# Kernel tuning notes

Measured on AMD Instinct MI355X. Metric: run time of the kernel, lower is better.

## Reference

```python
import jax, jax.numpy as jnp
import numpy as np

OUT_H, OUT_W = 512, 512
BATCH, CHANNELS = 64, 3


def setup_inputs() -> dict:
    key = jax.random.key(0)
    k1, k2 = jax.random.split(key)
    U = jax.random.normal(k1, (BATCH, OUT_H, OUT_W, CHANNELS), dtype=jnp.float32)
    theta = jax.random.normal(k2, (BATCH, 1), dtype=jnp.float32)
    return {"U": U, "theta": theta}


def reference(U, theta):
    B = U.shape[0]
    H, W = OUT_H, OUT_W
    # normalized sampling grid [H*W, 3] with homogeneous coordinate
    gx, gy = jnp.meshgrid(jnp.linspace(-1.0, 1.0, W), jnp.linspace(-1.0, 1.0, H))
    grid = jnp.stack([gx, gy, jnp.ones_like(gx)], axis=-1).reshape(H * W, 3)
    # rotation-only affine matrix [B, 2, 3]
    cos_t, sin_t, z = jnp.cos(theta), jnp.sin(theta), jnp.zeros_like(theta)
    rot = jnp.concatenate([cos_t, -sin_t, z, sin_t, cos_t, z], axis=1).reshape(B, 2, 3)
    # transformed source coords [B, H*W, 2]
    T_g = jnp.einsum('bij,nj->bni', rot, grid)
    x = (T_g[..., 0] + 1.0) * (W - 1) / 2.0
    y = (T_g[..., 1] + 1.0) * (H - 1) / 2.0
    x0f = jnp.floor(x).astype(jnp.int32)
    y0f = jnp.floor(y).astype(jnp.int32)
    x0 = jnp.clip(x0f, 0, W - 1)
    x1 = jnp.clip(x0f + 1, 0, W - 1)
    y0 = jnp.clip(y0f, 0, H - 1)
    y1 = jnp.clip(y0f + 1, 0, H - 1)
    # 4-corner gathers, batched: [B, H*W, C]
    gather = jax.vmap(lambda u, yy, xx: u[yy, xx])
    Ia = gather(U, y0, x0)
    Ib = gather(U, y1, x0)
    Ic = gather(U, y0, x1)
    Id = gather(U, y1, x1)
    x0_f, x1_f = x0.astype(jnp.float32), x1.astype(jnp.float32)
    y0_f, y1_f = y0.astype(jnp.float32), y1.astype(jnp.float32)
    wa = (x1_f - x) * (y1_f - y)
    wb = (x1_f - x) * (y - y0_f)
    wc = (x - x0_f) * (y1_f - y)
    wd = (x - x0_f) * (y - y0_f)
    out = (wa[..., None] * Ia + wb[..., None] * Ib
           + wc[..., None] * Ic + wd[..., None] * Id)
    return out.reshape(B, H, W, -1)
```

## Files before the change

### kernel.cpp

```cpp
#include <hip/hip_runtime.h>
#include <hip/hip_fp16.h>

#define OUT_H 512
#define OUT_W 512
#define BATCH 64
#define CHANS 3

#define WROWS 48
#define WPX   48
#define LPITCH 50
#define LSLOTS (WROWS * LPITCH)
#define IDX_MAX 2348

__global__ __launch_bounds__(256) void st_bilinear_kernel(
    const float* __restrict__ U,
    const float* __restrict__ theta,
    float* __restrict__ out)
{
    __shared__ __align__(16) unsigned int smA[LSLOTS];
    __shared__ __align__(16) unsigned int smB[LSLOTS];

    int blk  = blockIdx.x;
    int lblk = (blk & 7) * 2048 + (blk >> 3);

    int b  = lblk >> 8;
    int t  = lblk & 255;
    int i0 = (t >> 4) << 5;
    int j0 = (t & 15) << 5;

    int tid = threadIdx.x;

    float tt = theta[b];
    float s, c;
    __sincosf(tt, &s, &c);

    const float scale = 2.0f / 511.0f;
    float gx0 = (float)j0 * scale - 1.0f;
    float gy0 = (float)i0 * scale - 1.0f;
    float xb0 = (c * gx0 - s * gy0 + 1.0f) * 255.5f;
    float yb0 = (s * gx0 + c * gy0 + 1.0f) * 255.5f;

    float xmin = xb0 + fminf(0.0f, 31.0f * c) + fminf(0.0f, -31.0f * s);
    float ymin = yb0 + fminf(0.0f, 31.0f * s) + fminf(0.0f,  31.0f * c);

    int bx0 = min(max((int)floorf(xmin), 0), OUT_W - 1);
    int by0 = min(max((int)floorf(ymin), 0), OUT_H - 1);
    int bx_load = min(bx0, OUT_W - WPX);
    int by_load = min(by0, OUT_H - WROWS);

    const float* Ub = U + (size_t)b * (OUT_H * OUT_W * CHANS);
    const float* gb = Ub + ((size_t)by_load * OUT_W + bx_load) * CHANS;

    float4 va[5];
    float2 vb[5];
#pragma unroll
    for (int it = 0; it < 5; ++it) {
        unsigned P = (unsigned)tid + 256u * it;
        if (it < 4 || tid < 128) {
            unsigned r  = P / 24u;
            unsigned pr = P - r * 24u;
            const float* p = gb + (size_t)r * (OUT_W * CHANS) + pr * 6u;
            va[it] = *(const float4*)p;
            vb[it] = *(const float2*)(p + 4);
        }
    }
#pragma unroll
    for (int it = 0; it < 5; ++it) {
        unsigned P = (unsigned)tid + 256u * it;
        if (it < 4 || tid < 128) {
            unsigned r  = P / 24u;
            unsigned pr = P - r * 24u;
            unsigned slot = r * LPITCH + pr * 2u;
            float4 v = va[it]; float2 w = vb[it];
            __half2 ha0 = __floats2half2_rn(v.x, v.y);
            __half2 hb0 = __floats2half2_rn(v.z, 0.0f);
            __half2 ha1 = __floats2half2_rn(v.w, w.x);
            __half2 hb1 = __floats2half2_rn(w.y, 0.0f);
            uint2 wa, wb;
            wa.x = *(unsigned int*)&ha0; wa.y = *(unsigned int*)&ha1;
            wb.x = *(unsigned int*)&hb0; wb.y = *(unsigned int*)&hb1;
            *(uint2*)(smA + slot) = wa;
            *(uint2*)(smB + slot) = wb;
        }
    }
    __syncthreads();

    int il = tid >> 3;
    int jb = (tid & 7) << 2;
    float ilf = (float)il;
    float xr = xb0 - s * ilf;
    float yr = yb0 + c * ilf;
    int Koff = by_load * LPITCH + bx_load;

    float o[12];
#pragma unroll
    for (int p = 0; p < 4; ++p) {
        float jlf = (float)(jb + p);
        float x = fmaf(c, jlf, xr);
        float y = fmaf(s, jlf, yr);

        int ix = __float2int_rd(x);
        int iy = __float2int_rd(y);
        float fx = x - (float)ix;
        float fy = y - (float)iy;

        int idx = iy * LPITCH + ix - Koff;
        idx = min(max(idx, 0), IDX_MAX);

        unsigned iA0 = smA[idx],          iA1 = smA[idx + 1];
        unsigned iA2 = smA[idx + LPITCH], iA3 = smA[idx + LPITCH + 1];
        unsigned iB0 = smB[idx],          iB1 = smB[idx + 1];
        unsigned iB2 = smB[idx + LPITCH], iB3 = smB[idx + LPITCH + 1];

        __half2 fx2 = __float2half2_rn(fx);
        __half2 fy2 = __float2half2_rn(fy);
        __half2 A0 = *(__half2*)&iA0, A1 = *(__half2*)&iA1;
        __half2 A2 = *(__half2*)&iA2, A3 = *(__half2*)&iA3;
        __half2 B0 = *(__half2*)&iB0, B1 = *(__half2*)&iB1;
        __half2 B2 = *(__half2*)&iB2, B3 = *(__half2*)&iB3;

        __half2 tA = __hfma2(fx2, __hsub2(A1, A0), A0);
        __half2 bA = __hfma2(fx2, __hsub2(A3, A2), A2);
        __half2 rA = __hfma2(fy2, __hsub2(bA, tA), tA);
        __half2 tB = __hfma2(fx2, __hsub2(B1, B0), B0);
        __half2 bB = __hfma2(fx2, __hsub2(B3, B2), B2);
        __half2 rB = __hfma2(fy2, __hsub2(bB, tB), tB);

        bool valid = (x >= 0.0f) && (x < 511.0f) && (y >= 0.0f) && (y < 511.0f);
        o[p * 3 + 0] = valid ? __low2float(rA)  : 0.0f;
        o[p * 3 + 1] = valid ? __high2float(rA) : 0.0f;
        o[p * 3 + 2] = valid ? __low2float(rB)  : 0.0f;
    }

    float* po = out + (((size_t)b * OUT_H + (i0 + il)) * OUT_W + (j0 + jb)) * CHANS;
    ((float4*)po)[0] = make_float4(o[0], o[1], o[2],  o[3]);
    ((float4*)po)[1] = make_float4(o[4], o[5], o[6],  o[7]);
    ((float4*)po)[2] = make_float4(o[8], o[9], o[10], o[11]);
}

extern "C" void kernel_launch(void* const* d_in, const int* in_sizes, int n_in,
                              void* d_out, int out_size, void* d_ws, size_t ws_size,
                              hipStream_t stream) {
    const float* U     = (const float*)d_in[0];
    const float* theta = (const float*)d_in[1];
    float* out = (float*)d_out;

    int blocks = BATCH * (OUT_H / 32) * (OUT_W / 32);
    st_bilinear_kernel<<<blocks, 256, 0, stream>>>(U, theta, out);
}
```

Baseline: 103.4 us.

## Stage fp32 interleaved RGB tile in LDS instead of split fp16 planes

Replaces the two fp16 LDS planes (RG and B) with a single fp32 tile that keeps the interleaved RGB layout, using an odd pitch of 139 floats and a slightly smaller 46x46 window. The staging loop becomes plain float4 global loads written directly as scalars, with no half conversion or packing. Bilinear interpolation runs in fp32 from 12 scalar LDS reads per pixel. This drops conversion ALU work and the fp16 precision loss, at the cost of more LDS reads per pixel and a smaller halo margin for the rotated footprint. It also makes the batch index wave-uniform when loading theta.

Result: slower. 108.0 us (+4.5%).

```diff
diff --git a/kernel.cpp b/kernel.cpp
--- a/kernel.cpp
+++ b/kernel.cpp
@@ -1,24 +1,23 @@
 #include <hip/hip_runtime.h>
-#include <hip/hip_fp16.h>
 
 #define OUT_H 512
 #define OUT_W 512
 #define BATCH 64
 #define CHANS 3
 
-#define WROWS 48
-#define WPX   48
-#define LPITCH 50
-#define LSLOTS (WROWS * LPITCH)
-#define IDX_MAX 2348
+#define WROWS 46
+#define WPX   46
+#define RDW   138
+#define PITCH 139
+#define LSZ   (WROWS * PITCH)
+#define IDXMAX 6249
 
 __global__ __launch_bounds__(256) void st_bilinear_kernel(
     const float* __restrict__ U,
     const float* __restrict__ theta,
     float* __restrict__ out)
 {
-    __shared__ __align__(16) unsigned int smA[LSLOTS];
-    __shared__ __align__(16) unsigned int smB[LSLOTS];
+    __shared__ float smf[LSZ];
 
     int blk  = blockIdx.x;
     int lblk = (blk & 7) * 2048 + (blk >> 3);
@@ -30,7 +29,7 @@
 
     int tid = threadIdx.x;
 
-    float tt = theta[b];
+    float tt = theta[__builtin_amdgcn_readfirstlane(b)];
     float s, c;
     __sincosf(tt, &s, &c);
 
@@ -51,85 +50,76 @@
     const float* Ub = U + (size_t)b * (OUT_H * OUT_W * CHANS);
     const float* gb = Ub + ((size_t)by_load * OUT_W + bx_load) * CHANS;
 
-    float4 va[5];
-    float2 vb[5];
+    float4 va[7];
 #pragma unroll
-    for (int it = 0; it < 5; ++it) {
-        unsigned P = (unsigned)tid + 256u * it;
-        if (it < 4 || tid < 128) {
-            unsigned r  = P / 24u;
-            unsigned pr = P - r * 24u;
-            const float* p = gb + (size_t)r * (OUT_W * CHANS) + pr * 6u;
-            va[it] = *(const float4*)p;
-            vb[it] = *(const float2*)(p + 4);
+    for (int it = 0; it < 7; ++it) {
+        int u = tid + 256 * it;
+        if (it < 6 || u < 46 * 35) {
+            int r  = u / 35;
+            int cc = u - r * 35;
+            int dw = min(4 * cc, 134);
+            va[it] = *(const float4*)(gb + (size_t)r * (OUT_W * CHANS) + dw);
         }
     }
 #pragma unroll
-    for (int it = 0; it < 5; ++it) {
-        unsigned P = (unsigned)tid + 256u * it;
-        if (it < 4 || tid < 128) {
-            unsigned r  = P / 24u;
-            unsigned pr = P - r * 24u;
-            unsigned slot = r * LPITCH + pr * 2u;
-            float4 v = va[it]; float2 w = vb[it];
-            __half2 ha0 = __floats2half2_rn(v.x, v.y);
-            __half2 hb0 = __floats2half2_rn(v.z, 0.0f);
-            __half2 ha1 = __floats2half2_rn(v.w, w.x);
-            __half2 hb1 = __floats2half2_rn(w.y, 0.0f);
-            uint2 wa, wb;
-            wa.x = *(unsigned int*)&ha0; wa.y = *(unsigned int*)&ha1;
-            wb.x = *(unsigned int*)&hb0; wb.y = *(unsigned int*)&hb1;
-            *(uint2*)(smA + slot) = wa;
-            *(uint2*)(smB + slot) = wb;
+    for (int it = 0; it < 7; ++it) {
+        int u = tid + 256 * it;
+        if (it < 6 || u < 46 * 35) {
+            int r  = u / 35;
+            int cc = u - r * 35;
+            int dw = min(4 * cc, 134);
+            int base = r * PITCH + dw;
+            float4 v = va[it];
+            if (cc < 34) {
+                smf[base + 0] = v.x; smf[base + 1] = v.y;
+                smf[base + 2] = v.z; smf[base + 3] = v.w;
+            } else {
+                smf[base + 2] = v.z; smf[base + 3] = v.w;
+            }
         }
     }
     __syncthreads();
 
     int il = tid >> 3;
     int jb = (tid & 7) << 2;
-    float ilf = (float)il;
-    float xr = xb0 - s * ilf;
-    float yr = yb0 + c * ilf;
-    int Koff = by_load * LPITCH + bx_load;
+    float xr = xb0 + c * (float)jb - s * (float)il;
+    float yr = yb0 + s * (float)jb + c * (float)il;
+    int Koff = by_load * PITCH + bx_load * 3;
 
     float o[12];
 #pragma unroll
     for (int p = 0; p < 4; ++p) {
-        float jlf = (float)(jb + p);
-        float x = fmaf(c, jlf, xr);
-        float y = fmaf(s, jlf, yr);
+        float x = fmaf(c, (float)p, xr);
+        float y = fmaf(s, (float)p, yr);
 
         int ix = __float2int_rd(x);
         int iy = __float2int_rd(y);
         float fx = x - (float)ix;
         float fy = y - (float)iy;
 
-        int idx = iy * LPITCH + ix - Koff;
-        idx = min(max(idx, 0), IDX_MAX);
+        int idx = iy * PITCH + ix * 3 - Koff;
+        idx = min(max(idx, 0), IDXMAX);
 
-        unsigned iA0 = smA[idx],          iA1 = smA[idx + 1];
-        unsigned iA2 = smA[idx + LPITCH], iA3 = smA[idx + LPITCH + 1];
-        unsigned iB0 = smB[idx],          iB1 = smB[idx + 1];
-        unsigned iB2 = smB[idx + LPITCH], iB3 = smB[idx + LPITCH + 1];
+        const float* lp = smf + idx;
+        float a0 = lp[0], a1 = lp[1], a2 = lp[2];
+        float c0 = lp[3], c1 = lp[4], c2 = lp[5];
+        float b0 = lp[PITCH + 0], b1 = lp[PITCH + 1], b2 = lp[PITCH + 2];
+        float d0 = lp[PITCH + 3], d1 = lp[PITCH + 4], d2 = lp[PITCH + 5];
 
-        __half2 fx2 = __float2half2_rn(fx);
-        __half2 fy2 = __float2half2_rn(fy);
-        __half2 A0 = *(__half2*)&iA0, A1 = *(__half2*)&iA1;
-        __half2 A2 = *(__half2*)&iA2, A3 = *(__half2*)&iA3;
-        __half2 B0 = *(__half2*)&iB0, B1 = *(__half2*)&iB1;
-        __half2 B2 = *(__half2*)&iB2, B3 = *(__half2*)&iB3;
-
-        __half2 tA = __hfma2(fx2, __hsub2(A1, A0), A0);
-        __half2 bA = __hfma2(fx2, __hsub2(A3, A2), A2);
-        __half2 rA = __hfma2(fy2, __hsub2(bA, tA), tA);
-        __half2 tB = __hfma2(fx2, __hsub2(B1, B0), B0);
-        __half2 bB = __hfma2(fx2, __hsub2(B3, B2), B2);
-        __half2 rB = __hfma2(fy2, __hsub2(bB, tB), tB);
+        float t0 = fmaf(fx, c0 - a0, a0);
+        float t1 = fmaf(fx, c1 - a1, a1);
+        float t2 = fmaf(fx, c2 - a2, a2);
+        float u0 = fmaf(fx, d0 - b0, b0);
+        float u1 = fmaf(fx, d1 - b1, b1);
+        float u2 = fmaf(fx, d2 - b2, b2);
+        float r0 = fmaf(fy, u0 - t0, t0);
+        float r1 = fmaf(fy, u1 - t1, t1);
+        float r2 = fmaf(fy, u2 - t2, t2);
 
         bool valid = (x >= 0.0f) && (x < 511.0f) && (y >= 0.0f) && (y < 511.0f);
-        o[p * 3 + 0] = valid ? __low2float(rA)  : 0.0f;
-        o[p * 3 + 1] = valid ? __high2float(rA) : 0.0f;
-        o[p * 3 + 2] = valid ? __low2float(rB)  : 0.0f;
+        o[p * 3 + 0] = valid ? r0 : 0.0f;
+        o[p * 3 + 1] = valid ? r1 : 0.0f;
+        o[p * 3 + 2] = valid ? r2 : 0.0f;
     }
 
     float* po = out + (((size_t)b * OUT_H + (i0 + il)) * OUT_W + (j0 + jb)) * CHANS;
```
